# Optimization experiments

Hardware: AMD Instinct MI355X
Metric: run time of the kernel (lower is better)

The kernel has to match this reference:

```python
import jax, jax.numpy as jnp
import numpy as np

MESH_SIZE = 0.01
TEMP = 0.001
T = 4096
HID = (16, 16, 16)


def _triangle_mesh():
    g = np.arange(-1.0, 1.0 + 1e-9, MESH_SIZE, dtype=np.float32)  # 201 pts
    A, B = np.meshgrid(g, g, indexing='ij')  # alpha rows, beta cols
    mask = A >= B                             # Preisach triangle alpha >= beta
    return A[mask].astype(np.float32), B[mask].astype(np.float32)  # [N], [N]


def _constrain(v, lo, hi):
    return lo + (hi - lo) * jax.nn.sigmoid(v)


def setup_inputs() -> dict:
    key = jax.random.key(0)
    ks = jax.random.split(key, 12)
    alpha_np, beta_np = _triangle_mesh()
    N = alpha_np.shape[0]  # 20301

    def xavier(k, fan_in, fan_out):
        b = np.sqrt(6.0 / (fan_in + fan_out)).astype(np.float32)
        return jax.random.uniform(k, (fan_in, fan_out), jnp.float32, -b, b)

    dims = (2,) + HID + (1,)
    params = {}
    for i in range(4):
        params[f'w{i+1}'] = xavier(ks[i], dims[i], dims[i + 1])
        params[f'b{i+1}'] = jnp.zeros((dims[i + 1],), jnp.float32)

    bound = np.sqrt(6.0 / (1 + N)).astype(np.float32)  # xavier_uniform on (1,N)
    init_state_raw = jax.random.uniform(ks[10], (N,), jnp.float32, -bound, bound)

    return dict(
        x=jax.random.normal(ks[11], (T,), jnp.float32),
        alpha_raw=jnp.asarray(alpha_np),
        beta_raw=jnp.asarray(beta_np),
        init_state_raw=init_state_raw,
        m_scale_raw=jnp.asarray(1.0, jnp.float32),
        m_offset_raw=jnp.asarray(1.0, jnp.float32),
        h_scale_raw=jnp.asarray(1.0, jnp.float32),
        **params,
    )


def _get_states(x, alpha, beta, s0, temp):
    # Soft Preisach relay: switch up where u>alpha, down where u<beta, else hold.
    def step(s, u):
        up = jax.nn.sigmoid((u - alpha) / temp)
        dn = jax.nn.sigmoid((beta - u) / temp)
        s_new = up - dn + (1.0 - up) * (1.0 - dn) * s
        return s_new, s_new
    _, states = jax.lax.scan(step, s0, x)
    return states  # [T, N]


def reference(x, alpha_raw, beta_raw, init_state_raw,
              w1, b1, w2, b2, w3, b3, w4, b4,
              m_scale_raw, m_offset_raw, h_scale_raw):
    alpha = alpha_raw  # ConstrainedParameter with no bounds -> identity
    beta = beta_raw
    s0 = jnp.tanh(init_state_raw)  # BinaryParameter (soft binary)

    states = _get_states(x, alpha, beta, s0, TEMP)  # [T, N]

    mesh = jnp.stack([alpha, beta], axis=1)  # [N, 2]
    h = jax.nn.relu(mesh @ w1 + b1)
    h = jax.nn.relu(h @ w2 + b2)
    h = jax.nn.relu(h @ w3 + b3)
    density = jax.nn.sigmoid(h @ w4 + b4)  # [N, 1]
    density = density.T  # [1, N]

    m = jnp.sum(density * states, axis=-1) / jnp.sum(density, axis=-1)  # [T]

    m_scale = _constrain(m_scale_raw, 0.0, 10.0)
    m_offset = _constrain(m_offset_raw, -10.0, 10.0)
    h_scale = _constrain(h_scale_raw, 0.0, 10.0)

    out = m_scale * m + m_offset + h_scale * x  # [T]
    return out, density, states
```

## Files before the change

### kernel.cpp

```cpp
#include <hip/hip_runtime.h>
#include <math.h>

#define NM 20301
#define TT 4096
#define NC 16
#define CH 256
#define NBLK 80
#define TPH 32
#define NPH (CH / TPH)
#define LOG2E_K 1442.69504f

__device__ __forceinline__ float wave_reduce_sum(float w) {
    #pragma unroll
    for (int off = 32; off > 0; off >>= 1)
        w += __shfl_down(w, off, 64);
    return w;
}

__global__ __launch_bounds__(256) void density_kernel(
    const float* __restrict__ alpha, const float* __restrict__ beta,
    const float* __restrict__ w1, const float* __restrict__ b1,
    const float* __restrict__ w2, const float* __restrict__ b2,
    const float* __restrict__ w3, const float* __restrict__ b3,
    const float* __restrict__ w4, const float* __restrict__ b4,
    float* __restrict__ density_out, float* __restrict__ densum)
{
    int n = blockIdx.x * 256 + threadIdx.x;
    bool valid = n < NM;
    int nn = valid ? n : NM - 1;
    float a = alpha[nn], b = beta[nn];

    float h1[16], h2[16], h3[16];
    #pragma unroll
    for (int j = 0; j < 16; j++) {
        float v = fmaf(a, w1[j], fmaf(b, w1[16 + j], b1[j]));
        h1[j] = fmaxf(v, 0.f);
    }
    #pragma unroll
    for (int j = 0; j < 16; j++) {
        float v = b2[j];
        #pragma unroll
        for (int k = 0; k < 16; k++) v = fmaf(h1[k], w2[k * 16 + j], v);
        h2[j] = fmaxf(v, 0.f);
    }
    #pragma unroll
    for (int j = 0; j < 16; j++) {
        float v = b3[j];
        #pragma unroll
        for (int k = 0; k < 16; k++) v = fmaf(h2[k], w3[k * 16 + j], v);
        h3[j] = fmaxf(v, 0.f);
    }
    float v = b4[0];
    #pragma unroll
    for (int k = 0; k < 16; k++) v = fmaf(h3[k], w4[k], v);
    float d = 1.f / (1.f + __expf(-v));

    if (valid) density_out[n] = d;
    float wsum = wave_reduce_sum(valid ? d : 0.f);
    if ((threadIdx.x & 63) == 0) unsafeAtomicAdd(densum, wsum);
}

__global__ __launch_bounds__(256) void chunk_compose_kernel(
    const float* __restrict__ x, const float* __restrict__ alpha,
    const float* __restrict__ beta,
    float* __restrict__ Abuf, float* __restrict__ Bbuf)
{
    __shared__ float xs[CH];
    int c = blockIdx.y;
    xs[threadIdx.x] = x[c * CH + threadIdx.x] * LOG2E_K;
    __syncthreads();

    int n = blockIdx.x * 256 + threadIdx.x;
    int nn = (n < NM) ? n : NM - 1;
    float ka = alpha[nn] * LOG2E_K;
    float kb = beta[nn] * LOG2E_K;

    float A = 0.f, B = 1.f;
    #pragma unroll 8
    for (int i = 0; i < CH; i++) {
        float ku = xs[i];
        float e1 = __builtin_amdgcn_exp2f(ka - ku);
        float e2 = __builtin_amdgcn_exp2f(ku - kb);
        float up = __builtin_amdgcn_rcpf(1.f + e1);
        float dn = __builtin_amdgcn_rcpf(1.f + e2);
        float aa = up - dn;
        float bb = (1.f - up) * (1.f - dn);
        A = fmaf(bb, A, aa);
        B *= bb;
    }
    if (n < NM) { Abuf[c * NM + n] = A; Bbuf[c * NM + n] = B; }
}

__global__ __launch_bounds__(256) void chunk_scan_kernel(
    const float* __restrict__ init_raw,
    const float* __restrict__ Abuf, const float* __restrict__ Bbuf,
    float* __restrict__ sstart)
{
    int n = blockIdx.x * 256 + threadIdx.x;
    if (n >= NM) return;
    float s = tanhf(init_raw[n]);
    #pragma unroll
    for (int c = 0; c < NC; c++) {
        sstart[c * NM + n] = s;
        s = fmaf(Bbuf[c * NM + n], s, Abuf[c * NM + n]);
    }
}

__global__ __launch_bounds__(256) void states_kernel(
    const float* __restrict__ x, const float* __restrict__ alpha,
    const float* __restrict__ beta, const float* __restrict__ density,
    const float* __restrict__ sstart,
    float* __restrict__ states, float* __restrict__ partials)
{
    __shared__ float xs[CH];
    __shared__ float tile[256 * (TPH + 1)];
    __shared__ float lds2[TPH * 9];

    int tid = threadIdx.x;
    int c = blockIdx.y;
    xs[tid] = x[c * CH + tid] * LOG2E_K;

    int n = blockIdx.x * 256 + tid;
    bool valid = n < NM;
    int nn = valid ? n : NM - 1;
    float ka = alpha[nn] * LOG2E_K;
    float kb = beta[nn] * LOG2E_K;
    float d  = valid ? density[n] : 0.f;
    float s  = sstart[c * NM + nn];
    __syncthreads();

    float* rowp  = states + (size_t)c * CH * NM + n;
    float* tslot = &tile[tid * (TPH + 1)];
    int tl = tid & 31;
    int g  = tid >> 5;

    for (int p = 0; p < NPH; p++) {
        #pragma unroll
        for (int j = 0; j < TPH; j++) {
            int i = p * TPH + j;
            float ku = xs[i];
            float e1 = __builtin_amdgcn_exp2f(ka - ku);
            float e2 = __builtin_amdgcn_exp2f(ku - kb);
            float up = __builtin_amdgcn_rcpf(1.f + e1);
            float dn = __builtin_amdgcn_rcpf(1.f + e2);
            float aa = up - dn;
            float bb = (1.f - up) * (1.f - dn);
            s = fmaf(bb, s, aa);
            if (valid) rowp[(size_t)i * NM] = s;
            tslot[j] = d * s;
        }
        __syncthreads();
        float acc = 0.f;
        #pragma unroll
        for (int k = 0; k < 32; k++)
            acc += tile[(g * 32 + k) * (TPH + 1) + tl];
        lds2[tl * 9 + g] = acc;
        __syncthreads();
        if (tid < TPH) {
            float v = 0.f;
            #pragma unroll
            for (int g2 = 0; g2 < 8; g2++) v += lds2[tid * 9 + g2];
            partials[(size_t)blockIdx.x * TT + c * CH + p * TPH + tid] = v;
        }
    }
}

__global__ __launch_bounds__(256) void finalize_kernel(
    const float* __restrict__ x, const float* __restrict__ partials,
    const float* __restrict__ densum,
    const float* __restrict__ msr, const float* __restrict__ mor,
    const float* __restrict__ hsr, float* __restrict__ out)
{
    int t = blockIdx.x * 256 + threadIdx.x;
    if (t >= TT) return;
    float acc = 0.f;
    for (int bx = 0; bx < NBLK; bx++)
        acc += partials[(size_t)bx * TT + t];
    float sig_ms = 1.f / (1.f + __expf(-msr[0]));
    float sig_mo = 1.f / (1.f + __expf(-mor[0]));
    float sig_hs = 1.f / (1.f + __expf(-hsr[0]));
    float m_scale  = 10.f * sig_ms;
    float m_offset = fmaf(20.f, sig_mo, -10.f);
    float h_scale  = 10.f * sig_hs;
    float m = acc / densum[0];
    out[t] = fmaf(m_scale, m, m_offset) + h_scale * x[t];
}

extern "C" void kernel_launch(void* const* d_in, const int* in_sizes, int n_in,
                              void* d_out, int out_size, void* d_ws, size_t ws_size,
                              hipStream_t stream)
{
    const float* x    = (const float*)d_in[0];
    const float* alpha= (const float*)d_in[1];
    const float* beta = (const float*)d_in[2];
    const float* init = (const float*)d_in[3];
    const float* msr  = (const float*)d_in[4];
    const float* mor  = (const float*)d_in[5];
    const float* hsr  = (const float*)d_in[6];
    const float* w1   = (const float*)d_in[7];
    const float* b1   = (const float*)d_in[8];
    const float* w2   = (const float*)d_in[9];
    const float* b2   = (const float*)d_in[10];
    const float* w3   = (const float*)d_in[11];
    const float* b3   = (const float*)d_in[12];
    const float* w4   = (const float*)d_in[13];
    const float* b4   = (const float*)d_in[14];

    float* out     = (float*)d_out;
    float* density = out + TT;
    float* states  = density + NM;

    float* densum   = (float*)d_ws;
    float* sstart   = densum + 256;
    float* partials = sstart + NC * NM + 48;

    float* Abuf = states;
    float* Bbuf = states + (size_t)NC * NM;

    hipMemsetAsync(densum, 0, sizeof(float), stream);

    density_kernel<<<dim3(NBLK), dim3(256), 0, stream>>>(
        alpha, beta, w1, b1, w2, b2, w3, b3, w4, b4, density, densum);

    chunk_compose_kernel<<<dim3(NBLK, NC), dim3(256), 0, stream>>>(
        x, alpha, beta, Abuf, Bbuf);

    chunk_scan_kernel<<<dim3(NBLK), dim3(256), 0, stream>>>(
        init, Abuf, Bbuf, sstart);

    states_kernel<<<dim3(NBLK, NC), dim3(256), 0, stream>>>(
        x, alpha, beta, density, sstart, states, partials);

    finalize_kernel<<<dim3(TT / 256), dim3(256), 0, stream>>>(
        x, partials, densum, msr, mor, hsr, out);
}
```

Before: 486.0 us.

## Replace block barriers with per-wave reductions and drop densum atomic/memset

In the states kernel, each wave now reduces its own 64 lanes' density-weighted states through a private LDS tile and a cross-half shuffle, writing per-wave partials. This replaces the two block-wide __syncthreads per phase with wave-local waitcnts. The density sum uses per-block partials summed in finalize instead of an atomic plus a memset launch. In exchange, finalize reads four times as many partial rows, and correctness leans on wave-level LDS ordering.

```diff
diff --git a/kernel.cpp b/kernel.cpp
--- a/kernel.cpp
+++ b/kernel.cpp
@@ -6,6 +6,8 @@
 #define NC 16
 #define CH 256
 #define NBLK 80
+#define NWAVE 4
+#define NPAR (NBLK*NWAVE)
 #define TPH 32
 #define NPH (CH / TPH)
 #define LOG2E_K 1442.69504f
@@ -23,7 +25,7 @@
     const float* __restrict__ w2, const float* __restrict__ b2,
     const float* __restrict__ w3, const float* __restrict__ b3,
     const float* __restrict__ w4, const float* __restrict__ b4,
-    float* __restrict__ density_out, float* __restrict__ densum)
+    float* __restrict__ density_out, float* __restrict__ densum_parts)
 {
     int n = blockIdx.x * 256 + threadIdx.x;
     bool valid = n < NM;
@@ -57,7 +59,11 @@
 
     if (valid) density_out[n] = d;
     float wsum = wave_reduce_sum(valid ? d : 0.f);
-    if ((threadIdx.x & 63) == 0) unsafeAtomicAdd(densum, wsum);
+    __shared__ float ws_[NWAVE];
+    if ((threadIdx.x & 63) == 0) ws_[threadIdx.x >> 6] = wsum;
+    __syncthreads();
+    if (threadIdx.x == 0)
+        densum_parts[blockIdx.x] = ws_[0] + ws_[1] + ws_[2] + ws_[3];
 }
 
 __global__ __launch_bounds__(256) void chunk_compose_kernel(
@@ -113,8 +119,7 @@
     float* __restrict__ states, float* __restrict__ partials)
 {
     __shared__ float xs[CH];
-    __shared__ float tile[256 * (TPH + 1)];
-    __shared__ float lds2[TPH * 9];
+    __shared__ float tile[NWAVE * 64 * 33];
 
     int tid = threadIdx.x;
     int c = blockIdx.y;
@@ -129,10 +134,12 @@
     float s  = sstart[c * NM + nn];
     __syncthreads();
 
+    int wv = tid >> 6, ln = tid & 63;
+    int tl = ln & 31, h = ln >> 5;
+    float* wtile = &tile[wv * 64 * 33];
+    float* tslot = &wtile[ln * 33];
     float* rowp  = states + (size_t)c * CH * NM + n;
-    float* tslot = &tile[tid * (TPH + 1)];
-    int tl = tid & 31;
-    int g  = tid >> 5;
+    size_t prow  = (size_t)(blockIdx.x * NWAVE + wv) * TT + c * CH;
 
     for (int p = 0; p < NPH; p++) {
         #pragma unroll
@@ -149,40 +156,38 @@
             if (valid) rowp[(size_t)i * NM] = s;
             tslot[j] = d * s;
         }
-        __syncthreads();
+        asm volatile("s_waitcnt lgkmcnt(0)" ::: "memory");
         float acc = 0.f;
         #pragma unroll
         for (int k = 0; k < 32; k++)
-            acc += tile[(g * 32 + k) * (TPH + 1) + tl];
-        lds2[tl * 9 + g] = acc;
-        __syncthreads();
-        if (tid < TPH) {
-            float v = 0.f;
-            #pragma unroll
-            for (int g2 = 0; g2 < 8; g2++) v += lds2[tid * 9 + g2];
-            partials[(size_t)blockIdx.x * TT + c * CH + p * TPH + tid] = v;
-        }
+            acc += wtile[(h * 32 + k) * 33 + tl];
+        acc += __shfl_xor(acc, 32, 64);
+        if (ln < 32) partials[prow + p * TPH + ln] = acc;
+        asm volatile("s_waitcnt lgkmcnt(0)" ::: "memory");
     }
 }
 
 __global__ __launch_bounds__(256) void finalize_kernel(
     const float* __restrict__ x, const float* __restrict__ partials,
-    const float* __restrict__ densum,
+    const float* __restrict__ densum_parts,
     const float* __restrict__ msr, const float* __restrict__ mor,
     const float* __restrict__ hsr, float* __restrict__ out)
 {
     int t = blockIdx.x * 256 + threadIdx.x;
     if (t >= TT) return;
     float acc = 0.f;
+    for (int r = 0; r < NPAR; r++)
+        acc += partials[(size_t)r * TT + t];
+    float dsum = 0.f;
     for (int bx = 0; bx < NBLK; bx++)
-        acc += partials[(size_t)bx * TT + t];
+        dsum += densum_parts[bx];
     float sig_ms = 1.f / (1.f + __expf(-msr[0]));
     float sig_mo = 1.f / (1.f + __expf(-mor[0]));
     float sig_hs = 1.f / (1.f + __expf(-hsr[0]));
     float m_scale  = 10.f * sig_ms;
     float m_offset = fmaf(20.f, sig_mo, -10.f);
     float h_scale  = 10.f * sig_hs;
-    float m = acc / densum[0];
+    float m = acc / dsum;
     out[t] = fmaf(m_scale, m, m_offset) + h_scale * x[t];
 }
 
@@ -210,17 +215,15 @@
     float* density = out + TT;
     float* states  = density + NM;
 
-    float* densum   = (float*)d_ws;
-    float* sstart   = densum + 256;
-    float* partials = sstart + NC * NM + 48;
+    float* densum_parts = (float*)d_ws;
+    float* sstart       = densum_parts + 128;
+    float* partials     = sstart + NC * NM;
 
     float* Abuf = states;
     float* Bbuf = states + (size_t)NC * NM;
 
-    hipMemsetAsync(densum, 0, sizeof(float), stream);
-
     density_kernel<<<dim3(NBLK), dim3(256), 0, stream>>>(
-        alpha, beta, w1, b1, w2, b2, w3, b3, w4, b4, density, densum);
+        alpha, beta, w1, b1, w2, b2, w3, b3, w4, b4, density, densum_parts);
 
     chunk_compose_kernel<<<dim3(NBLK, NC), dim3(256), 0, stream>>>(
         x, alpha, beta, Abuf, Bbuf);
@@ -232,5 +235,5 @@
         x, alpha, beta, density, sstart, states, partials);
 
     finalize_kernel<<<dim3(TT / 256), dim3(256), 0, stream>>>(
-        x, partials, densum, msr, mor, hsr, out);
-}
+        x, partials, densum_parts, msr, mor, hsr, out);
+}
```

New measurement: 493.3 us. About the same (+1.5%).
